# Kernel tuning notes

Measured on AMD Instinct MI355X. Metric: run time of the kernel, lower is better.

## Reference

```python
import jax, jax.numpy as jnp
import numpy as np

H = 12          # num_attention_heads
D = 64          # num_embed_hidden == attention_head_size
B, T = 4, 2048
SCALE = 1.0 / np.sqrt(D)


def setup_inputs() -> dict:
    key = jax.random.key(0)
    ks = jax.random.split(key, 7)
    P = H * D  # num_attn_proj = 768
    s = 1.0 / np.sqrt(D)
    return {
        "hidden_states": jax.random.normal(ks[0], (B, T, D), dtype=jnp.float32),
        "attention_mask": jnp.ones((B, T), dtype=jnp.float32),
        "Wq": jax.random.normal(ks[1], (D, P), dtype=jnp.float32) * s,
        "bq": jnp.zeros((P,), dtype=jnp.float32),
        "Wk": jax.random.normal(ks[2], (D, P), dtype=jnp.float32) * s,
        "bk": jnp.zeros((P,), dtype=jnp.float32),
        "Wv": jax.random.normal(ks[3], (D, P), dtype=jnp.float32) * s,
        "bv": jnp.zeros((P,), dtype=jnp.float32),
    }


def reference(hidden_states, attention_mask, Wq, bq, Wk, bk, Wv, bv):
    b, t, _ = hidden_states.shape
    # QKV projections -> [B, H, T, D]
    def proj(W, bias):
        return (hidden_states @ W + bias).reshape(b, t, H, D).transpose(0, 2, 1, 3)
    q = proj(Wq, bq)
    k = proj(Wk, bk)
    v = proj(Wv, bv)
    # [B, H, T, T] scores
    scores = jnp.einsum("bhqd,bhkd->bhqk", q, k) * SCALE
    mask = (1.0 - attention_mask)[:, None, None, :] * -10000.0
    scores = scores + mask
    attn = jax.nn.softmax(scores, axis=-1)
    # dropout is identity in eval mode
    y = jnp.einsum("bhqk,bhkd->bhqd", attn, v)
    return y.transpose(0, 2, 1, 3).reshape(b, t, H * D)
```

## Files before the change

kernel.cpp:

```cpp
#include <hip/hip_runtime.h>
#include <hip/hip_bf16.h>

#define NH 12
#define HD 64
#define NB 4
#define SEQ 2048
#define NP 768
#define LOG2E 1.44269504f
#define MASK_L2 14426.9504f

typedef __bf16 bf16x8 __attribute__((ext_vector_type(8)));
typedef __bf16 bf16x2 __attribute__((ext_vector_type(2)));
typedef float f32x2 __attribute__((ext_vector_type(2)));
typedef float f32x4 __attribute__((ext_vector_type(4)));
typedef float f32x16 __attribute__((ext_vector_type(16)));
typedef unsigned u32x4 __attribute__((ext_vector_type(4)));

static __device__ __forceinline__ bf16x8 load_bf16x8(const __bf16* p) {
    return *reinterpret_cast<const bf16x8*>(p);
}
static __device__ __forceinline__ float hw_exp2(float x) {
    return __builtin_amdgcn_exp2f(x);
}
static __device__ __forceinline__ unsigned cvtpk2(float lo, float hi) {
    f32x2 t; t[0] = lo; t[1] = hi;
    return __builtin_bit_cast(unsigned, __builtin_convertvector(t, bf16x2));
}

__global__ __launch_bounds__(256) void qkv_kernel(
    const float* __restrict__ hidden,
    const float* __restrict__ Wq, const float* __restrict__ Wk,
    const float* __restrict__ Wv,
    const float* __restrict__ bq, const float* __restrict__ bk,
    const float* __restrict__ bv,
    __bf16* __restrict__ Qw, __bf16* __restrict__ Kf, __bf16* __restrict__ Vf)
{
    __shared__ __bf16 wtileT[64][72];
    __shared__ __bf16 ot[64][72];

    const int tid  = threadIdx.x;
    const int lane = tid & 63;
    const int w    = tid >> 6;
    const int g    = lane >> 4;
    const int n    = lane & 15;
    const int n32  = lane & 31;
    const int hi   = lane >> 5;

    const int row0 = blockIdx.x * 64;
    const int gi   = blockIdx.y;
    const int b_   = row0 >> 11;
    const int t0   = row0 & (SEQ - 1);
    const int kb64 = t0 >> 6;

    const float* hrow = hidden + (size_t)(row0 + w * 16 + n) * HD + 8 * g;
    f32x4 h0 = *(const f32x4*)(hrow);
    f32x4 h1 = *(const f32x4*)(hrow + 4);
    f32x4 h2 = *(const f32x4*)(hrow + 32);
    f32x4 h3 = *(const f32x4*)(hrow + 36);
    bf16x8 a0, a1;
    #pragma unroll
    for (int j = 0; j < 4; ++j) {
        a0[j]     = (__bf16)h0[j];
        a0[j + 4] = (__bf16)h1[j];
        a1[j]     = (__bf16)h2[j];
        a1[j + 4] = (__bf16)h3[j];
    }

    const int dr   = tid >> 2;
    const int coff = (tid & 3) * 16;

    for (int tt = 0; tt < 6; ++tt) {
        const int tile_id = gi * 6 + tt;
        const int proj    = tile_id / 12;
        const int head    = tile_id % 12;
        const int bh      = b_ * NH + head;
        const float* W    = proj == 0 ? Wq : (proj == 1 ? Wk : Wv);
        const float* bias = proj == 0 ? bq : (proj == 1 ? bk : bv);
        const float qs    = (proj == 0) ? 0.125f * LOG2E : 1.0f;

        const float* wr = W + (size_t)dr * NP + head * 64 + coff;
        f32x4 x0 = *(const f32x4*)(wr);
        f32x4 x1 = *(const f32x4*)(wr + 4);
        f32x4 x2 = *(const f32x4*)(wr + 8);
        f32x4 x3 = *(const f32x4*)(wr + 12);
        #pragma unroll
        for (int i = 0; i < 4; ++i) {
            wtileT[coff + i     ][dr] = (__bf16)(x0[i] * qs);
            wtileT[coff + 4 + i ][dr] = (__bf16)(x1[i] * qs);
            wtileT[coff + 8 + i ][dr] = (__bf16)(x2[i] * qs);
            wtileT[coff + 12 + i][dr] = (__bf16)(x3[i] * qs);
        }
        __syncthreads();

        #pragma unroll
        for (int dt = 0; dt < 4; ++dt) {
            const bf16x8 b0 = *(const bf16x8*)&wtileT[dt * 16 + n][8 * g];
            const bf16x8 b1 = *(const bf16x8*)&wtileT[dt * 16 + n][32 + 8 * g];
            f32x4 acc = {0.f, 0.f, 0.f, 0.f};
            acc = __builtin_amdgcn_mfma_f32_16x16x32_bf16(a0, b0, acc, 0, 0, 0);
            acc = __builtin_amdgcn_mfma_f32_16x16x32_bf16(a1, b1, acc, 0, 0, 0);
            const float bb = bias[head * 64 + dt * 16 + n] * qs;
            #pragma unroll
            for (int r = 0; r < 4; ++r)
                ot[w * 16 + 4 * g + r][dt * 16 + n] = (__bf16)(acc[r] + bb);
        }
        __syncthreads();

        if (proj == 0) {
            __bf16* dst = Qw + ((size_t)bh * SEQ + t0 + w * 16) * HD;
            const int tr = lane >> 2;
            const int d0 = (lane & 3) * 16;
            *(bf16x8*)(dst + (size_t)tr * HD + d0)     = *(const bf16x8*)&ot[w * 16 + tr][d0];
            *(bf16x8*)(dst + (size_t)tr * HD + d0 + 8) = *(const bf16x8*)&ot[w * 16 + tr][d0 + 8];
        } else if (proj == 1) {
            __bf16* base = Kf + (size_t)bh * SEQ * HD + (size_t)kb64 * 4096;
            #pragma unroll
            for (int sub = 0; sub < 2; ++sub) {
                const bf16x8 fr = *(const bf16x8*)&ot[sub * 32 + n32][w * 16 + 8 * hi];
                *(bf16x8*)(base + (size_t)(w * 2 + sub) * 512 + lane * 8) = fr;
            }
        } else {
            __bf16* base = Vf + (size_t)bh * SEQ * HD + (size_t)kb64 * 4096;
            #pragma unroll
            for (int dsub = 0; dsub < 2; ++dsub) {
                bf16x8 v;
                #pragma unroll
                for (int j = 0; j < 8; ++j)
                    v[j] = ot[w * 16 + ((j & 3) + 8 * (j >> 2) + 4 * hi)][dsub * 32 + n32];
                *(bf16x8*)(base + (size_t)(w * 2 + dsub) * 512 + lane * 8) = v;
            }
        }
    }
}

__global__ __launch_bounds__(256, 4) void flash_attn_kernel(
    const __bf16* __restrict__ Qw, const __bf16* __restrict__ Kf,
    const __bf16* __restrict__ Vf, const float* __restrict__ amask,
    float* __restrict__ out)
{
    __shared__ __align__(16) float et[4][32][68];
    __shared__ float lrow[4][32];
    __shared__ __bf16 mdd[SEQ];

    const int tid  = threadIdx.x;
    const int lane = tid & 63;
    const int w    = tid >> 6;
    const int n32  = lane & 31;
    const int hi   = lane >> 5;

    const int bid    = blockIdx.x;
    const int xcd    = bid & 7;
    const int slot   = bid >> 3;
    const int bh     = xcd * 6 + (slot >> 6);
    const int qchunk = slot & 63;
    const int b_     = bh / NH;
    const int h      = bh % NH;
    const int q0     = qchunk * 32;

    const float* mp = amask + (size_t)b_ * SEQ;
    #pragma unroll
    for (int i = 0; i < 8; ++i) {
        const int idx = w * 512 + i * 64 + lane;
        mdd[idx] = (__bf16)fmaf(mp[idx], MASK_L2, -MASK_L2);
    }

    const __bf16* Qrow = Qw + ((size_t)bh * SEQ + q0 + n32) * HD + 8 * hi;
    bf16x8 qf[4];
    #pragma unroll
    for (int d = 0; d < 4; ++d) qf[d] = load_bf16x8(Qrow + d * 16);

    bf16x8 qone;
    #pragma unroll
    for (int j = 0; j < 8; ++j) qone[j] = (__bf16)0.0f;
    if (hi == 0) qone[0] = (__bf16)1.0f;

    const __bf16* kfb_ = Kf + (size_t)bh * SEQ * HD + (size_t)lane * 8;
    const __bf16* vfb_ = Vf + (size_t)bh * SEQ * HD + (size_t)lane * 8;

    f32x16 o0 = {0,0,0,0,0,0,0,0,0,0,0,0,0,0,0,0};
    f32x16 o1 = {0,0,0,0,0,0,0,0,0,0,0,0,0,0,0,0};
    f32x2 lsl2 = {0.f, 0.f};

    const int kstart = w * 512;

    bf16x8 kca[4], kcb[4];
    {
        const size_t f0 = (size_t)(kstart >> 6) * 4096;
        #pragma unroll
        for (int d = 0; d < 4; ++d) {
            kca[d] = load_bf16x8(kfb_ + f0 + (size_t)(2 * d) * 512);
            kcb[d] = load_bf16x8(kfb_ + f0 + (size_t)(2 * d + 1) * 512);
        }
    }

    for (int it = 0; it < 8; ++it) {
        const int kb = kstart + it * 64;
        const size_t foff = (size_t)(kb >> 6) * 4096;
        const int nkb = (kb + 64) & (SEQ - 1);
        const size_t nfoff = (size_t)(nkb >> 6) * 4096;

        bf16x8 vf0[4], vf1[4];
        #pragma unroll
        for (int c = 0; c < 4; ++c) {
            vf0[c] = load_bf16x8(vfb_ + foff + (size_t)(2 * c) * 512);
            vf1[c] = load_bf16x8(vfb_ + foff + (size_t)(2 * c + 1) * 512);
        }
        bf16x8 kna[4], knb[4];
        #pragma unroll
        for (int d = 0; d < 4; ++d) {
            kna[d] = load_bf16x8(kfb_ + nfoff + (size_t)(2 * d) * 512);
            knb[d] = load_bf16x8(kfb_ + nfoff + (size_t)(2 * d + 1) * 512);
        }

        bf16x8 maa, mab;
        #pragma unroll
        for (int j = 0; j < 8; ++j) { maa[j] = (__bf16)0.0f; mab[j] = (__bf16)0.0f; }
        maa[0] = mdd[kb + n32];
        mab[0] = mdd[kb + 32 + n32];

        f32x16 sa = {0,0,0,0,0,0,0,0,0,0,0,0,0,0,0,0};
        f32x16 sb = {0,0,0,0,0,0,0,0,0,0,0,0,0,0,0,0};
        #pragma unroll
        for (int d = 0; d < 4; ++d)
            sa = __builtin_amdgcn_mfma_f32_32x32x16_bf16(kca[d], qf[d], sa, 0, 0, 0);
        sa = __builtin_amdgcn_mfma_f32_32x32x16_bf16(maa, qone, sa, 0, 0, 0);
        #pragma unroll
        for (int d = 0; d < 4; ++d)
            sb = __builtin_amdgcn_mfma_f32_32x32x16_bf16(kcb[d], qf[d], sb, 0, 0, 0);
        sb = __builtin_amdgcn_mfma_f32_32x32x16_bf16(mab, qone, sb, 0, 0, 0);

        bf16x8 P0, P1;
        {
            float p[16];
            #pragma unroll
            for (int r = 0; r < 16; ++r) p[r] = hw_exp2(sa[r]);
            u32x4 B0, B1;
            #pragma unroll
            for (int i = 0; i < 4; ++i) {
                B0[i] = cvtpk2(p[2 * i],     p[2 * i + 1]);
                B1[i] = cvtpk2(p[8 + 2 * i], p[8 + 2 * i + 1]);
            }
            #pragma unroll
            for (int i = 0; i < 8; ++i) {
                f32x2 t; t[0] = p[2 * i]; t[1] = p[2 * i + 1];
                lsl2 += t;
            }
            P0 = __builtin_bit_cast(bf16x8, B0);
            P1 = __builtin_bit_cast(bf16x8, B1);
        }
        o0 = __builtin_amdgcn_mfma_f32_32x32x16_bf16(vf0[0], P0, o0, 0, 0, 0);
        o1 = __builtin_amdgcn_mfma_f32_32x32x16_bf16(vf1[0], P0, o1, 0, 0, 0);
        o0 = __builtin_amdgcn_mfma_f32_32x32x16_bf16(vf0[1], P1, o0, 0, 0, 0);
        o1 = __builtin_amdgcn_mfma_f32_32x32x16_bf16(vf1[1], P1, o1, 0, 0, 0);

        bf16x8 P2, P3;
        {
            float p[16];
            #pragma unroll
            for (int r = 0; r < 16; ++r) p[r] = hw_exp2(sb[r]);
            u32x4 B0, B1;
            #pragma unroll
            for (int i = 0; i < 4; ++i) {
                B0[i] = cvtpk2(p[2 * i],     p[2 * i + 1]);
                B1[i] = cvtpk2(p[8 + 2 * i], p[8 + 2 * i + 1]);
            }
            #pragma unroll
            for (int i = 0; i < 8; ++i) {
                f32x2 t; t[0] = p[2 * i]; t[1] = p[2 * i + 1];
                lsl2 += t;
            }
            P2 = __builtin_bit_cast(bf16x8, B0);
            P3 = __builtin_bit_cast(bf16x8, B1);
        }
        o0 = __builtin_amdgcn_mfma_f32_32x32x16_bf16(vf0[2], P2, o0, 0, 0, 0);
        o1 = __builtin_amdgcn_mfma_f32_32x32x16_bf16(vf1[2], P2, o1, 0, 0, 0);
        o0 = __builtin_amdgcn_mfma_f32_32x32x16_bf16(vf0[3], P3, o0, 0, 0, 0);
        o1 = __builtin_amdgcn_mfma_f32_32x32x16_bf16(vf1[3], P3, o1, 0, 0, 0);

        #pragma unroll
        for (int d = 0; d < 4; ++d) { kca[d] = kna[d]; kcb[d] = knb[d]; }
    }

    float rs = lsl2[0] + lsl2[1];
    rs += __shfl_xor(rs, 32);

    #pragma unroll
    for (int r = 0; r < 16; ++r) {
        const int dl = (r & 3) + 8 * (r >> 2) + 4 * hi;
        et[w][n32][dl]      = o0[r];
        et[w][n32][32 + dl] = o1[r];
    }
    if (lane < 32) lrow[w][n32] = rs;
    __syncthreads();

    const int q  = tid >> 3;
    const int d0 = (tid & 7) * 8;
    const float linv = 1.0f / (lrow[0][q] + lrow[1][q] + lrow[2][q] + lrow[3][q]);
    f32x4 acc0 = {0,0,0,0}, acc1 = {0,0,0,0};
    #pragma unroll
    for (int ww = 0; ww < 4; ++ww) {
        acc0 += *(const f32x4*)&et[ww][q][d0];
        acc1 += *(const f32x4*)&et[ww][q][d0 + 4];
    }
    float* orow = out + ((size_t)(b_ * SEQ + q0 + q)) * NP + h * HD + d0;
    f32x4 r0, r1;
    #pragma unroll
    for (int i = 0; i < 4; ++i) { r0[i] = acc0[i] * linv; r1[i] = acc1[i] * linv; }
    *(f32x4*)(orow)     = r0;
    *(f32x4*)(orow + 4) = r1;
}

extern "C" void kernel_launch(void* const* d_in, const int* in_sizes, int n_in,
                              void* d_out, int out_size, void* d_ws, size_t ws_size,
                              hipStream_t stream) {
    const float* hidden = (const float*)d_in[0];
    const float* amask  = (const float*)d_in[1];
    const float* Wq     = (const float*)d_in[2];
    const float* bq     = (const float*)d_in[3];
    const float* Wk     = (const float*)d_in[4];
    const float* bk     = (const float*)d_in[5];
    const float* Wv     = (const float*)d_in[6];
    const float* bv     = (const float*)d_in[7];
    float* out = (float*)d_out;

    const size_t elems = (size_t)NB * NH * SEQ * HD;
    __bf16* Qw = (__bf16*)d_ws;
    __bf16* Kf = Qw + elems;
    __bf16* Vf = Kf + elems;

    qkv_kernel<<<dim3(128, 6), 256, 0, stream>>>(
        hidden, Wq, Wk, Wv, bq, bk, bv, Qw, Kf, Vf);

    flash_attn_kernel<<<dim3(3072), 256, 0, stream>>>(
        Qw, Kf, Vf, amask, out);
}
```

Before: 167.9 us.

## Share K/V tiles via async LDS double buffering across waves with distinct query rows

Measured after the change: 158.9 us. -5.4%, faster.

```diff
diff --git a/kernel.cpp b/kernel.cpp
--- a/kernel.cpp
+++ b/kernel.cpp
@@ -25,6 +25,11 @@
 static __device__ __forceinline__ unsigned cvtpk2(float lo, float hi) {
     f32x2 t; t[0] = lo; t[1] = hi;
     return __builtin_bit_cast(unsigned, __builtin_convertvector(t, bf16x2));
+}
+static __device__ __forceinline__ void async16(const __bf16* g, __bf16* l) {
+    __builtin_amdgcn_global_load_lds(
+        (const __attribute__((address_space(1))) unsigned*)(g),
+        (__attribute__((address_space(3))) unsigned*)(l), 16, 0, 0);
 }
 
 __global__ __launch_bounds__(256) void qkv_kernel(
@@ -133,13 +138,15 @@
     }
 }
 
-__global__ __launch_bounds__(256, 4) void flash_attn_kernel(
+__global__ __launch_bounds__(256, 3) void flash_attn_kernel(
     const __bf16* __restrict__ Qw, const __bf16* __restrict__ Kf,
     const __bf16* __restrict__ Vf, const float* __restrict__ amask,
     float* __restrict__ out)
 {
-    __shared__ __align__(16) float et[4][32][68];
-    __shared__ float lrow[4][32];
+    __shared__ __align__(16) union {
+        __bf16 kv[2][8192];
+        float  et[4][32][68];
+    } u;
     __shared__ __bf16 mdd[SEQ];
 
     const int tid  = threadIdx.x;
@@ -148,14 +155,14 @@
     const int n32  = lane & 31;
     const int hi   = lane >> 5;
 
-    const int bid    = blockIdx.x;
-    const int xcd    = bid & 7;
-    const int slot   = bid >> 3;
-    const int bh     = xcd * 6 + (slot >> 6);
-    const int qchunk = slot & 63;
-    const int b_     = bh / NH;
-    const int h      = bh % NH;
-    const int q0     = qchunk * 32;
+    const int bid  = blockIdx.x;
+    const int xcd  = bid & 7;
+    const int slot = bid >> 3;
+    const int bh   = xcd * 6 + (slot >> 4);
+    const int qblk = slot & 15;
+    const int b_   = bh / NH;
+    const int h    = bh % NH;
+    const int q0   = qblk * 128 + w * 32;
 
     const float* mp = amask + (size_t)b_ * SEQ;
     #pragma unroll
@@ -174,42 +181,37 @@
     for (int j = 0; j < 8; ++j) qone[j] = (__bf16)0.0f;
     if (hi == 0) qone[0] = (__bf16)1.0f;
 
-    const __bf16* kfb_ = Kf + (size_t)bh * SEQ * HD + (size_t)lane * 8;
-    const __bf16* vfb_ = Vf + (size_t)bh * SEQ * HD + (size_t)lane * 8;
+    const size_t bhoff = (size_t)bh * SEQ * HD;
+    const __bf16* gbase = (w < 2 ? Kf : Vf) + bhoff + (w & 1) * 2048 + (size_t)lane * 8;
+    __bf16* const lbase = &u.kv[0][0] + ((w & 2) ? 4096 : 0) + (w & 1) * 2048;
+
+    #pragma unroll
+    for (int c = 0; c < 4; ++c) async16(gbase + c * 512, lbase + c * 512);
+    __syncthreads();
 
     f32x16 o0 = {0,0,0,0,0,0,0,0,0,0,0,0,0,0,0,0};
     f32x16 o1 = {0,0,0,0,0,0,0,0,0,0,0,0,0,0,0,0};
     f32x2 lsl2 = {0.f, 0.f};
 
-    const int kstart = w * 512;
-
-    bf16x8 kca[4], kcb[4];
-    {
-        const size_t f0 = (size_t)(kstart >> 6) * 4096;
+    for (int it = 0; it < 32; ++it) {
+        const int cur = it & 1;
+        const int kb  = it << 6;
+
+        {
+            const __bf16* s = gbase + (size_t)((it + 1) & 31) * 4096;
+            __bf16* dl = lbase + (cur ^ 1) * 8192;
+            #pragma unroll
+            for (int c = 0; c < 4; ++c) async16(s + c * 512, dl + c * 512);
+        }
+
+        const __bf16* Kb = &u.kv[cur][0];
+        const __bf16* Vb = Kb + 4096;
+
+        bf16x8 kca[4], kcb[4];
         #pragma unroll
         for (int d = 0; d < 4; ++d) {
-            kca[d] = load_bf16x8(kfb_ + f0 + (size_t)(2 * d) * 512);
-            kcb[d] = load_bf16x8(kfb_ + f0 + (size_t)(2 * d + 1) * 512);
-        }
-    }
-
-    for (int it = 0; it < 8; ++it) {
-        const int kb = kstart + it * 64;
-        const size_t foff = (size_t)(kb >> 6) * 4096;
-        const int nkb = (kb + 64) & (SEQ - 1);
-        const size_t nfoff = (size_t)(nkb >> 6) * 4096;
-
-        bf16x8 vf0[4], vf1[4];
-        #pragma unroll
-        for (int c = 0; c < 4; ++c) {
-            vf0[c] = load_bf16x8(vfb_ + foff + (size_t)(2 * c) * 512);
-            vf1[c] = load_bf16x8(vfb_ + foff + (size_t)(2 * c + 1) * 512);
-        }
-        bf16x8 kna[4], knb[4];
-        #pragma unroll
-        for (int d = 0; d < 4; ++d) {
-            kna[d] = load_bf16x8(kfb_ + nfoff + (size_t)(2 * d) * 512);
-            knb[d] = load_bf16x8(kfb_ + nfoff + (size_t)(2 * d + 1) * 512);
+            kca[d] = load_bf16x8(Kb + (2 * d) * 512 + lane * 8);
+            kcb[d] = load_bf16x8(Kb + (2 * d + 1) * 512 + lane * 8);
         }
 
         bf16x8 maa, mab;
@@ -220,6 +222,7 @@
 
         f32x16 sa = {0,0,0,0,0,0,0,0,0,0,0,0,0,0,0,0};
         f32x16 sb = {0,0,0,0,0,0,0,0,0,0,0,0,0,0,0,0};
+        __builtin_amdgcn_s_setprio(1);
         #pragma unroll
         for (int d = 0; d < 4; ++d)
             sa = __builtin_amdgcn_mfma_f32_32x32x16_bf16(kca[d], qf[d], sa, 0, 0, 0);
@@ -228,6 +231,14 @@
         for (int d = 0; d < 4; ++d)
             sb = __builtin_amdgcn_mfma_f32_32x32x16_bf16(kcb[d], qf[d], sb, 0, 0, 0);
         sb = __builtin_amdgcn_mfma_f32_32x32x16_bf16(mab, qone, sb, 0, 0, 0);
+        __builtin_amdgcn_s_setprio(0);
+
+        bf16x8 vf0[4], vf1[4];
+        #pragma unroll
+        for (int c = 0; c < 4; ++c) {
+            vf0[c] = load_bf16x8(Vb + (2 * c) * 512 + lane * 8);
+            vf1[c] = load_bf16x8(Vb + (2 * c + 1) * 512 + lane * 8);
+        }
 
         bf16x8 P0, P1;
         {
@@ -248,10 +259,12 @@
             P0 = __builtin_bit_cast(bf16x8, B0);
             P1 = __builtin_bit_cast(bf16x8, B1);
         }
+        __builtin_amdgcn_s_setprio(1);
         o0 = __builtin_amdgcn_mfma_f32_32x32x16_bf16(vf0[0], P0, o0, 0, 0, 0);
         o1 = __builtin_amdgcn_mfma_f32_32x32x16_bf16(vf1[0], P0, o1, 0, 0, 0);
         o0 = __builtin_amdgcn_mfma_f32_32x32x16_bf16(vf0[1], P1, o0, 0, 0, 0);
         o1 = __builtin_amdgcn_mfma_f32_32x32x16_bf16(vf1[1], P1, o1, 0, 0, 0);
+        __builtin_amdgcn_s_setprio(0);
 
         bf16x8 P2, P3;
         {
@@ -272,42 +285,41 @@
             P2 = __builtin_bit_cast(bf16x8, B0);
             P3 = __builtin_bit_cast(bf16x8, B1);
         }
+        __builtin_amdgcn_s_setprio(1);
         o0 = __builtin_amdgcn_mfma_f32_32x32x16_bf16(vf0[2], P2, o0, 0, 0, 0);
         o1 = __builtin_amdgcn_mfma_f32_32x32x16_bf16(vf1[2], P2, o1, 0, 0, 0);
         o0 = __builtin_amdgcn_mfma_f32_32x32x16_bf16(vf0[3], P3, o0, 0, 0, 0);
         o1 = __builtin_amdgcn_mfma_f32_32x32x16_bf16(vf1[3], P3, o1, 0, 0, 0);
-
-        #pragma unroll
-        for (int d = 0; d < 4; ++d) { kca[d] = kna[d]; kcb[d] = knb[d]; }
+        __builtin_amdgcn_s_setprio(0);
+
+        __syncthreads();
     }
 
     float rs = lsl2[0] + lsl2[1];
     rs += __shfl_xor(rs, 32);
 
     #pragma unroll
-    for (int r = 0; r < 16; ++r) {
-        const int dl = (r & 3) + 8 * (r >> 2) + 4 * hi;
-        et[w][n32][dl]      = o0[r];
-        et[w][n32][32 + dl] = o1[r];
-    }
-    if (lane < 32) lrow[w][n32] = rs;
-    __syncthreads();
-
-    const int q  = tid >> 3;
-    const int d0 = (tid & 7) * 8;
-    const float linv = 1.0f / (lrow[0][q] + lrow[1][q] + lrow[2][q] + lrow[3][q]);
-    f32x4 acc0 = {0,0,0,0}, acc1 = {0,0,0,0};
-    #pragma unroll
-    for (int ww = 0; ww < 4; ++ww) {
-        acc0 += *(const f32x4*)&et[ww][q][d0];
-        acc1 += *(const f32x4*)&et[ww][q][d0 + 4];
-    }
-    float* orow = out + ((size_t)(b_ * SEQ + q0 + q)) * NP + h * HD + d0;
-    f32x4 r0, r1;
-    #pragma unroll
-    for (int i = 0; i < 4; ++i) { r0[i] = acc0[i] * linv; r1[i] = acc1[i] * linv; }
-    *(f32x4*)(orow)     = r0;
-    *(f32x4*)(orow + 4) = r1;
+    for (int k = 0; k < 4; ++k) {
+        f32x4 t0, t1;
+        #pragma unroll
+        for (int j = 0; j < 4; ++j) { t0[j] = o0[4 * k + j]; t1[j] = o1[4 * k + j]; }
+        *(f32x4*)&u.et[w][n32][8 * k + 4 * hi]      = t0;
+        *(f32x4*)&u.et[w][n32][32 + 8 * k + 4 * hi] = t1;
+    }
+    const int d0 = (lane & 7) * 8;
+    #pragma unroll
+    for (int pass = 0; pass < 4; ++pass) {
+        const int q = pass * 8 + (lane >> 3);
+        const float linv = 1.0f / __shfl(rs, q);
+        const float* er = &u.et[w][q][d0];
+        f32x4 r0 = *(const f32x4*)(er);
+        f32x4 r1 = *(const f32x4*)(er + 4);
+        #pragma unroll
+        for (int i = 0; i < 4; ++i) { r0[i] *= linv; r1[i] *= linv; }
+        float* orow = out + ((size_t)b_ * SEQ + q0 + q) * NP + h * HD + d0;
+        *(f32x4*)(orow)     = r0;
+        *(f32x4*)(orow + 4) = r1;
+    }
 }
 
 extern "C" void kernel_launch(void* const* d_in, const int* in_sizes, int n_in,
@@ -331,6 +343,6 @@
     qkv_kernel<<<dim3(128, 6), 256, 0, stream>>>(
         hidden, Wq, Wk, Wv, bq, bk, bv, Qw, Kf, Vf);
 
-    flash_attn_kernel<<<dim3(3072), 256, 0, stream>>>(
+    flash_attn_kernel<<<dim3(768), 256, 0, stream>>>(
         Qw, Kf, Vf, amask, out);
 }
```
